# Optimization experiments

Measured on AMD Instinct MI355X. Metric: run time of the kernel, lower is better.

Reference implementation:

```python
import jax, jax.numpy as jnp
import numpy as np

B, S, H, NH, DK = 128, 512, 1000, 8, 125
LN_EPS = 1e-5


def setup_inputs() -> dict:
    key = jax.random.key(0)
    ks = jax.random.split(key, 12)
    s = 1.0 / np.sqrt(H)
    inp = {
        "q": jax.random.normal(ks[0], (B, S, H), jnp.float32),
        "k": jax.random.normal(ks[1], (B, S, H), jnp.float32),
        "v": jax.random.normal(ks[2], (B, S, H), jnp.float32),
        "mask": jax.random.randint(ks[3], (B, 1, 1, S), 0, 2) > 0,
        "Wq_w": jax.random.normal(ks[4], (H, H), jnp.float32) * s,
        "Wq_b": jnp.zeros((H,), jnp.float32),
        "Wk_w": jax.random.normal(ks[5], (H, H), jnp.float32) * s,
        "Wk_b": jnp.zeros((H,), jnp.float32),
        "Wv_w": jax.random.normal(ks[6], (H, H), jnp.float32) * s,
        "Wv_b": jnp.zeros((H,), jnp.float32),
        "Wo_w": jax.random.normal(ks[7], (H, H), jnp.float32) * s,
        "Wo_b": jnp.zeros((H,), jnp.float32),
        "ln_g": jnp.ones((H,), jnp.float32),
        "ln_b": jnp.zeros((H,), jnp.float32),
    }
    return inp


def _layernorm(x, g, b):
    mu = jnp.mean(x, -1, keepdims=True)
    var = jnp.mean(jnp.square(x - mu), -1, keepdims=True)
    return (x - mu) * jax.lax.rsqrt(var + LN_EPS) * g + b


def reference(q, k, v, mask, Wq_w, Wq_b, Wk_w, Wk_b, Wv_w, Wv_b, Wo_w, Wo_b, ln_g, ln_b):
    x = q
    # projections: torch Linear is x @ W.T + b
    qh = (q @ Wq_w.T + Wq_b).reshape(B, S, NH, DK).transpose(0, 2, 1, 3)  # [B,NH,S,DK]
    kh = (k @ Wk_w.T + Wk_b).reshape(B, S, NH, DK).transpose(0, 2, 1, 3)
    vh = (v @ Wv_w.T + Wv_b).reshape(B, S, NH, DK).transpose(0, 2, 1, 3)
    scores = jnp.einsum("bhqd,bhkd->bhqk", qh, kh) / np.sqrt(DK)  # [B,NH,S,S]
    scores = jnp.where(mask, jnp.float32(-10000.0), scores)
    a = jax.nn.softmax(scores, axis=-1)
    z = jnp.einsum("bhqk,bhkd->bhqd", a, vh)  # [B,NH,S,DK]
    z = z.transpose(0, 2, 1, 3).reshape(B, S, NH * DK)
    z = z @ Wo_w.T + Wo_b
    # dropout is identity in eval mode
    return _layernorm(x + z, ln_g, ln_b)
```

## Files before the change

### kernel.cpp

```cpp
#include <hip/hip_runtime.h>


typedef unsigned short u16;
typedef short short8 __attribute__((ext_vector_type(8)));
typedef float f32x4 __attribute__((ext_vector_type(8/2)));

#define XQ_E 0ull
#define XK_E 67108864ull
#define XV_E 134217728ull
#define WQ_E 201326592ull
#define WK_E 202375168ull
#define WV_E 203423744ull
#define WO_E 204472320ull
#define QH_E 205520896ull
#define KH_E 272629760ull
#define VT_E 339738624ull
#define Z2_E 0ull
#define Y_BYTE 134217728ull

__device__ __forceinline__ u16 f2bf(float f) {
  unsigned u = __float_as_uint(f);
  u += 0x7fffu + ((u >> 16) & 1u);
  return (u16)(u >> 16);
}

__device__ __forceinline__ void gl_lds16(const void* g, void* l) {
  __builtin_amdgcn_global_load_lds((const __attribute__((address_space(1))) void*)g,
                                   (__attribute__((address_space(3))) void*)l,
                                   16, 0, 0);
}

__global__ __launch_bounds__(128) void cvt_kernel(
    const float* __restrict__ q, const float* __restrict__ k, const float* __restrict__ v,
    const float* __restrict__ wq, const float* __restrict__ wk,
    const float* __restrict__ wv, const float* __restrict__ wo,
    u16* __restrict__ ws16) {
  const int row = blockIdx.x;
  const int c0 = threadIdx.x * 8;
  const float* src;
  u16* dst;
  bool valid;
  if (row < 196608) {
    const int m = row >> 16, r = row & 65535;
    src = (m == 0 ? q : (m == 1 ? k : v)) + (size_t)r * 1000;
    dst = ws16 + (size_t)m * 67108864ull + (size_t)r * 1024;
    valid = (c0 < 1000);
  } else {
    const int t2 = row - 196608;
    const int wm = t2 >> 10, r = t2 & 1023;
    const float* W = (wm == 0 ? wq : (wm == 1 ? wk : (wm == 2 ? wv : wo)));
    src = W + (size_t)r * 1000;
    dst = ws16 + WQ_E + (size_t)wm * 1048576ull + (size_t)r * 1024;
    valid = (c0 < 1000) && (r < 1000);
  }
  short8 o = {0, 0, 0, 0, 0, 0, 0, 0};
  if (valid) {
    float4 a = *(const float4*)(src + c0);
    float4 b = *(const float4*)(src + c0 + 4);
    o[0] = (short)f2bf(a.x); o[1] = (short)f2bf(a.y);
    o[2] = (short)f2bf(a.z); o[3] = (short)f2bf(a.w);
    o[4] = (short)f2bf(b.x); o[5] = (short)f2bf(b.y);
    o[6] = (short)f2bf(b.z); o[7] = (short)f2bf(b.w);
  }
  *(short8*)(dst + c0) = o;
}

__global__ __launch_bounds__(256) void zpad_kernel(u16* __restrict__ ws16) {
  const int r = blockIdx.x * 256 + threadIdx.x;
  u16* p = ws16 + KH_E + (size_t)r * 128 + 125;
  p[0] = 0; p[1] = 0; p[2] = 0;
}

__global__ __launch_bounds__(256, 2) void gemm_bt(
    u16* __restrict__ ws16,
    const float* __restrict__ bq, const float* __restrict__ bk,
    const float* __restrict__ bv, const float* __restrict__ bo,
    const float* __restrict__ qres, int mode_base) {
  const int mode = mode_base + blockIdx.z;
  const u16* A; const u16* Bw; const float* bias;
  if (mode == 0)      { A = ws16 + XQ_E; Bw = ws16 + WQ_E; bias = bq; }
  else if (mode == 1) { A = ws16 + XK_E; Bw = ws16 + WK_E; bias = bk; }
  else if (mode == 2) { A = ws16 + XV_E; Bw = ws16 + WV_E; bias = bv; }
  else                { A = ws16 + Z2_E; Bw = ws16 + WO_E; bias = bo; }

  __shared__ __attribute__((aligned(16))) u16 lA[128 * 64];
  __shared__ __attribute__((aligned(16))) u16 lB[128 * 64];

  const int tid = threadIdx.x;
  const int w = tid >> 6, lane = tid & 63;
  const int m0 = blockIdx.x * 128, n0 = blockIdx.y * 128;

  const f32x4 zz = {0.f, 0.f, 0.f, 0.f};
  f32x4 acc[4][4];
#pragma unroll
  for (int mi = 0; mi < 4; ++mi)
#pragma unroll
    for (int ni = 0; ni < 4; ++ni) acc[mi][ni] = zz;

  const int srow = lane >> 3;
  const int scol = (lane & 7) * 8;
  const int wm = (w >> 1) * 64, wn = (w & 1) * 64;
  const int fr = lane & 15, quad = lane >> 4, fq = quad * 8;

  for (int kt = 0; kt < 16; ++kt) {
    __syncthreads();
    const int k0 = kt * 64;
#pragma unroll
    for (int i = 0; i < 4; ++i) {
      const int rbase = w * 32 + i * 8;
      gl_lds16(A  + (size_t)(m0 + rbase + srow) * 1024 + k0 + scol, (void*)(lA + rbase * 64));
      gl_lds16(Bw + (size_t)(n0 + rbase + srow) * 1024 + k0 + scol, (void*)(lB + rbase * 64));
    }
    __syncthreads();
#pragma unroll
    for (int ks = 0; ks < 2; ++ks) {
      short8 af[4], bf[4];
#pragma unroll
      for (int mi = 0; mi < 4; ++mi)
        af[mi] = *(const short8*)(lA + (wm + mi * 16 + fr) * 64 + ks * 32 + fq);
#pragma unroll
      for (int ni = 0; ni < 4; ++ni)
        bf[ni] = *(const short8*)(lB + (wn + ni * 16 + fr) * 64 + ks * 32 + fq);
#pragma unroll
      for (int mi = 0; mi < 4; ++mi)
#pragma unroll
        for (int ni = 0; ni < 4; ++ni)
          acc[mi][ni] = __builtin_amdgcn_mfma_f32_16x16x32_bf16(af[mi], bf[ni], acc[mi][ni], 0, 0, 0);
    }
  }

#pragma unroll
  for (int mi = 0; mi < 4; ++mi)
#pragma unroll
    for (int ni = 0; ni < 4; ++ni)
#pragma unroll
      for (int r = 0; r < 4; ++r) {
        const int gr = m0 + wm + mi * 16 + quad * 4 + r;
        const int gc = n0 + wn + ni * 16 + fr;
        if (gc >= 1000) continue;
        float val = acc[mi][ni][r] + bias[gc];
        if (mode <= 1) {
          if (mode == 0) val *= 0.08944271909999159f;
          const int head = gc / 125, dk = gc - head * 125;
          const int b = gr >> 9, s = gr & 511;
          u16* dst = ws16 + (mode == 0 ? QH_E : KH_E);
          dst[((size_t)((b * 8 + head) * 512 + s)) * 128 + dk] = f2bf(val);
        } else if (mode == 2) {
          const int head = gc / 125, dk = gc - head * 125;
          const int b = gr >> 9, s = gr & 511;
          ws16[VT_E + ((size_t)((b * 8 + head) * 128 + dk)) * 512 + s] = f2bf(val);
        } else {
          float* Y = (float*)((char*)ws16 + Y_BYTE);
          Y[(size_t)gr * 1000 + gc] = val + qres[(size_t)gr * 1000 + gc];
        }
      }
}

__global__ __launch_bounds__(256, 2) void attn_kernel(
    u16* __restrict__ ws16, const int* __restrict__ maskp) {
  const u16* QH = ws16 + QH_E;
  const u16* KH = ws16 + KH_E;
  const u16* VT = ws16 + VT_E;
  u16* Z2 = ws16 + Z2_E;

  const int qt = blockIdx.x, bnh = blockIdx.y;
  const int b = bnh >> 3, head = bnh & 7;
  const int tid = threadIdx.x, w = tid >> 6, lane = tid & 63;
  const int fr = lane & 15, quad = lane >> 4, fq = quad * 8;

  __shared__ __attribute__((aligned(16))) u16 lQ[64 * 128];
  __shared__ __attribute__((aligned(16))) u16 lKV[64 * 128];
  __shared__ __attribute__((aligned(16))) u16 lP[4][16 * 72];
  __shared__ float lM[512];

  {
    const int* mp = maskp + b * 512;
    lM[tid] = mp[tid] ? 1.0f : 0.0f;
    lM[tid + 256] = mp[tid + 256] ? 1.0f : 0.0f;
  }
  {
    const int lrow = lane >> 4, lc = (lane & 15) * 8;
#pragma unroll
    for (int i = 0; i < 4; ++i) {
      const int rbase = w * 16 + i * 4;
      gl_lds16(QH + ((size_t)(bnh * 512 + qt * 64 + rbase + lrow)) * 128 + lc,
               (void*)(lQ + rbase * 128));
    }
  }
  __syncthreads();

  short8 af[4];
#pragma unroll
  for (int ks = 0; ks < 4; ++ks)
    af[ks] = *(const short8*)(lQ + (w * 16 + fr) * 128 + ks * 32 + fq);

  const f32x4 zz = {0.f, 0.f, 0.f, 0.f};
  f32x4 sA[32];
#pragma unroll
  for (int i = 0; i < 32; ++i) sA[i] = zz;

#pragma unroll
  for (int kt = 0; kt < 8; ++kt) {
    __syncthreads();
    {
      const int lrow = lane >> 4, lc = (lane & 15) * 8;
#pragma unroll
      for (int i = 0; i < 4; ++i) {
        const int rbase = w * 16 + i * 4;
        gl_lds16(KH + ((size_t)(bnh * 512 + kt * 64 + rbase + lrow)) * 128 + lc,
                 (void*)(lKV + rbase * 128));
      }
    }
    __syncthreads();
#pragma unroll
    for (int ks = 0; ks < 4; ++ks)
#pragma unroll
      for (int n = 0; n < 4; ++n) {
        short8 bf = *(const short8*)(lKV + (n * 16 + fr) * 128 + ks * 32 + fq);
        sA[kt * 4 + n] = __builtin_amdgcn_mfma_f32_16x16x32_bf16(af[ks], bf, sA[kt * 4 + n], 0, 0, 0);
      }
  }

  float linv[4];
#pragma unroll
  for (int r = 0; r < 4; ++r) {
    float mr = -3.0e38f;
#pragma unroll
    for (int ct = 0; ct < 32; ++ct) {
      float vv = sA[ct][r];
      vv = (lM[ct * 16 + fr] != 0.0f) ? -10000.0f : vv;
      sA[ct][r] = vv;
      mr = fmaxf(mr, vv);
    }
    mr = fmaxf(mr, __shfl_xor(mr, 1, 64));
    mr = fmaxf(mr, __shfl_xor(mr, 2, 64));
    mr = fmaxf(mr, __shfl_xor(mr, 4, 64));
    mr = fmaxf(mr, __shfl_xor(mr, 8, 64));
    float lr = 0.f;
#pragma unroll
    for (int ct = 0; ct < 32; ++ct) {
      float p = __expf(sA[ct][r] - mr);
      sA[ct][r] = p;
      lr += p;
    }
    lr += __shfl_xor(lr, 1, 64);
    lr += __shfl_xor(lr, 2, 64);
    lr += __shfl_xor(lr, 4, 64);
    lr += __shfl_xor(lr, 8, 64);
    linv[r] = 1.0f / lr;
  }

  f32x4 zA[8];
#pragma unroll
  for (int n = 0; n < 8; ++n) zA[n] = zz;
  u16* myP = lP[w];

#pragma unroll
  for (int kt = 0; kt < 8; ++kt) {
    __syncthreads();
    {
      const int lrow = lane >> 3, lc = (lane & 7) * 8;
#pragma unroll
      for (int i = 0; i < 4; ++i) {
        const int rbase = w * 32 + i * 8;
        gl_lds16(VT + ((size_t)(bnh * 128 + rbase + lrow)) * 512 + kt * 64 + lc,
                 (void*)(lKV + rbase * 64));
      }
    }
    __syncthreads();
#pragma unroll
    for (int n = 0; n < 4; ++n)
#pragma unroll
      for (int r = 0; r < 4; ++r)
        myP[(quad * 4 + r) * 72 + n * 16 + fr] = f2bf(sA[kt * 4 + n][r]);
#pragma unroll
    for (int ks = 0; ks < 2; ++ks) {
      short8 ap = *(const short8*)(myP + fr * 72 + ks * 32 + fq);
#pragma unroll
      for (int n = 0; n < 8; ++n) {
        short8 bv = *(const short8*)(lKV + (n * 16 + fr) * 64 + ks * 32 + fq);
        zA[n] = __builtin_amdgcn_mfma_f32_16x16x32_bf16(ap, bv, zA[n], 0, 0, 0);
      }
    }
  }

#pragma unroll
  for (int n = 0; n < 8; ++n)
#pragma unroll
    for (int r = 0; r < 4; ++r) {
      const int dk = n * 16 + fr;
      if (dk < 125) {
        const int sg = qt * 64 + w * 16 + quad * 4 + r;
        const float val = zA[n][r] * linv[r];
        Z2[((size_t)(b * 512 + sg)) * 1024 + head * 125 + dk] = f2bf(val);
      }
    }
}

__global__ __launch_bounds__(256) void ln_kernel(
    const float* __restrict__ Y, const float* __restrict__ g,
    const float* __restrict__ be, float* __restrict__ out) {
  const size_t row = blockIdx.x;
  const int t = threadIdx.x;
  const float* yr = Y + row * 1000;
  float4 x = make_float4(0.f, 0.f, 0.f, 0.f);
  if (t < 250) x = *(const float4*)(yr + t * 4);
  float s1 = x.x + x.y + x.z + x.w;
  float s2 = x.x * x.x + x.y * x.y + x.z * x.z + x.w * x.w;
#pragma unroll
  for (int off = 1; off < 64; off <<= 1) {
    s1 += __shfl_xor(s1, off, 64);
    s2 += __shfl_xor(s2, off, 64);
  }
  __shared__ float r1[4], r2[4];
  const int w = t >> 6, lane = t & 63;
  if (lane == 0) { r1[w] = s1; r2[w] = s2; }
  __syncthreads();
  const float S1 = r1[0] + r1[1] + r1[2] + r1[3];
  const float S2 = r2[0] + r2[1] + r2[2] + r2[3];
  const float mu = S1 * 0.001f;
  const float var = S2 * 0.001f - mu * mu;
  const float rstd = rsqrtf(var + 1e-5f);
  if (t < 250) {
    float4 gg = *(const float4*)(g + t * 4);
    float4 bb = *(const float4*)(be + t * 4);
    float4 o;
    o.x = (x.x - mu) * rstd * gg.x + bb.x;
    o.y = (x.y - mu) * rstd * gg.y + bb.y;
    o.z = (x.z - mu) * rstd * gg.z + bb.z;
    o.w = (x.w - mu) * rstd * gg.w + bb.w;
    *(float4*)(out + row * 1000 + t * 4) = o;
  }
}

extern "C" void kernel_launch(void* const* d_in, const int* in_sizes, int n_in,
                              void* d_out, int out_size, void* d_ws, size_t ws_size,
                              hipStream_t stream) {
  const float* q   = (const float*)d_in[0];
  const float* k   = (const float*)d_in[1];
  const float* v   = (const float*)d_in[2];
  const int*   mk  = (const int*)  d_in[3];
  const float* wqw = (const float*)d_in[4];
  const float* wqb = (const float*)d_in[5];
  const float* wkw = (const float*)d_in[6];
  const float* wkb = (const float*)d_in[7];
  const float* wvw = (const float*)d_in[8];
  const float* wvb = (const float*)d_in[9];
  const float* wow = (const float*)d_in[10];
  const float* wob = (const float*)d_in[11];
  const float* lng = (const float*)d_in[12];
  const float* lnb = (const float*)d_in[13];
  u16* ws16 = (u16*)d_ws;

  cvt_kernel<<<dim3(200704), dim3(128), 0, stream>>>(q, k, v, wqw, wkw, wvw, wow, ws16);
  zpad_kernel<<<dim3(2048), dim3(256), 0, stream>>>(ws16);
  gemm_bt<<<dim3(512, 8, 3), dim3(256), 0, stream>>>(ws16, wqb, wkb, wvb, wob, q, 0);
  attn_kernel<<<dim3(8, 1024), dim3(256), 0, stream>>>(ws16, mk);
  gemm_bt<<<dim3(512, 8, 1), dim3(256), 0, stream>>>(ws16, wqb, wkb, wvb, wob, q, 3);
  ln_kernel<<<dim3(65536), dim3(256), 0, stream>>>(
      (const float*)((const char*)d_ws + Y_BYTE), lng, lnb, (float*)d_out);
}
```

Measured before the change: 2.481 ms.

## Rewrite projection GEMM with 256x256 tiles, double-buffered swizzled LDS and prefetch

The projection GEMM moves from 128x128 tiles with 256 threads to 256x256 tiles with 512 threads. LDS is double-buffered, global-to-LDS loads for the next K step are interleaved with MFMA work using explicit waitcnt and barriers, and LDS uses an XOR swizzle to avoid bank conflicts. Block indices are remapped so neighbouring blocks share tiles, which should improve L2 reuse. The goal is to hide load latency and raise MFMA utilisation, at the cost of much more LDS (128 KB per block), more registers for accumulators, and fragile hand-tuned vmcnt counts.

```diff
diff --git a/kernel.cpp b/kernel.cpp
--- a/kernel.cpp
+++ b/kernel.cpp
@@ -3,7 +3,7 @@
 
 typedef unsigned short u16;
 typedef short short8 __attribute__((ext_vector_type(8)));
-typedef float f32x4 __attribute__((ext_vector_type(8/2)));
+typedef float f32x4 __attribute__((ext_vector_type(4)));
 
 #define XQ_E 0ull
 #define XK_E 67108864ull
@@ -71,7 +71,7 @@
   p[0] = 0; p[1] = 0; p[2] = 0;
 }
 
-__global__ __launch_bounds__(256, 2) void gemm_bt(
+__global__ __launch_bounds__(512, 2) void gemm_bt(
     u16* __restrict__ ws16,
     const float* __restrict__ bq, const float* __restrict__ bk,
     const float* __restrict__ bv, const float* __restrict__ bo,
@@ -83,60 +83,111 @@
   else if (mode == 2) { A = ws16 + XV_E; Bw = ws16 + WV_E; bias = bv; }
   else                { A = ws16 + Z2_E; Bw = ws16 + WO_E; bias = bo; }
 
-  __shared__ __attribute__((aligned(16))) u16 lA[128 * 64];
-  __shared__ __attribute__((aligned(16))) u16 lB[128 * 64];
+  __shared__ __attribute__((aligned(16))) u16 lA[2][256 * 64];
+  __shared__ __attribute__((aligned(16))) u16 lB[2][256 * 64];
 
   const int tid = threadIdx.x;
-  const int w = tid >> 6, lane = tid & 63;
-  const int m0 = blockIdx.x * 128, n0 = blockIdx.y * 128;
+  const int wid = tid >> 6, lane = tid & 63;
+  const int wr = wid >> 2, wc = wid & 3;
+  const int fr = lane & 15, quad = lane >> 4;
+  const int widl = wid * 512;
+
+  const int f = blockIdx.x;
+  const int logical = (f & 7) * 128 + (f >> 3);
+  const int mt = logical >> 2, nt = logical & 3;
+  const int m0 = mt * 256, n0 = nt * 256;
+
+  const int r8 = tid >> 3;
+  const int swz_cb = ((tid & 7) * 16) ^ ((r8 & 7) << 4);
+  const char* srcA = (const char*)(A + (size_t)m0 * 1024) + (size_t)r8 * 2048 + swz_cb;
+  const char* srcB = (const char*)(Bw + (size_t)n0 * 1024) + (size_t)r8 * 2048 + swz_cb;
+
+  auto stA = [&](int b2, int q, int kb) {
+    gl_lds16(srcA + (size_t)q * 131072 + kb, (void*)(&lA[b2][q * 4096 + widl]));
+  };
+  auto stB = [&](int b2, int q, int kb) {
+    gl_lds16(srcB + (size_t)q * 131072 + kb, (void*)(&lB[b2][q * 4096 + widl]));
+  };
 
   const f32x4 zz = {0.f, 0.f, 0.f, 0.f};
-  f32x4 acc[4][4];
-#pragma unroll
-  for (int mi = 0; mi < 4; ++mi)
+  f32x4 acc[8][4];
+#pragma unroll
+  for (int mi = 0; mi < 8; ++mi)
 #pragma unroll
     for (int ni = 0; ni < 4; ++ni) acc[mi][ni] = zz;
 
-  const int srow = lane >> 3;
-  const int scol = (lane & 7) * 8;
-  const int wm = (w >> 1) * 64, wn = (w & 1) * 64;
-  const int fr = lane & 15, quad = lane >> 4, fq = quad * 8;
-
-  for (int kt = 0; kt < 16; ++kt) {
-    __syncthreads();
-    const int k0 = kt * 64;
-#pragma unroll
-    for (int i = 0; i < 4; ++i) {
-      const int rbase = w * 32 + i * 8;
-      gl_lds16(A  + (size_t)(m0 + rbase + srow) * 1024 + k0 + scol, (void*)(lA + rbase * 64));
-      gl_lds16(Bw + (size_t)(n0 + rbase + srow) * 1024 + k0 + scol, (void*)(lB + rbase * 64));
-    }
-    __syncthreads();
-#pragma unroll
-    for (int ks = 0; ks < 2; ++ks) {
-      short8 af[4], bf[4];
-#pragma unroll
-      for (int mi = 0; mi < 4; ++mi)
-        af[mi] = *(const short8*)(lA + (wm + mi * 16 + fr) * 64 + ks * 32 + fq);
-#pragma unroll
-      for (int ni = 0; ni < 4; ++ni)
-        bf[ni] = *(const short8*)(lB + (wn + ni * 16 + fr) * 64 + ks * 32 + fq);
-#pragma unroll
-      for (int mi = 0; mi < 4; ++mi)
+  stB(0, 0, 0); stB(0, 1, 0); stB(0, 2, 0); stB(0, 3, 0);
+  stA(0, 0, 0); stA(0, 2, 0); stA(0, 1, 0); stA(0, 3, 0);
+  asm volatile("s_waitcnt vmcnt(2)" ::: "memory");
+  asm volatile("s_barrier" ::: "memory");
+
+  const int rowA = (wr * 128 + fr) * 128;
+  const int rowB = (wc * 64 + fr) * 128;
+  const int swr = (fr & 7) << 4;
+
+  short8 bfr[4][2];
+
+#pragma unroll 2
+  for (int t = 0; t < 16; ++t) {
+    const int buf = t & 1, nb = buf ^ 1;
+    const char* tA = (const char*)(&lA[buf][0]);
+    const char* tB = (const char*)(&lB[buf][0]);
+    const int kb = (t + 1) * 128;
+    const bool pf = (t < 15);
+
+#pragma unroll
+    for (int p = 0; p < 4; ++p) {
+      short8 afr[2][2];
+#pragma unroll
+      for (int j = 0; j < 2; ++j)
+#pragma unroll
+        for (int ks = 0; ks < 2; ++ks)
+          afr[j][ks] = *(const short8*)(tA + rowA + (p * 2 + j) * 2048 +
+                                        ((ks * 64 + quad * 16) ^ swr));
+      if (p == 0) {
 #pragma unroll
         for (int ni = 0; ni < 4; ++ni)
-          acc[mi][ni] = __builtin_amdgcn_mfma_f32_16x16x32_bf16(af[mi], bf[ni], acc[mi][ni], 0, 0, 0);
-    }
-  }
-
-#pragma unroll
-  for (int mi = 0; mi < 4; ++mi)
+#pragma unroll
+          for (int ks = 0; ks < 2; ++ks)
+            bfr[ni][ks] = *(const short8*)(tB + rowB + ni * 2048 +
+                                           ((ks * 64 + quad * 16) ^ swr));
+      }
+      if (pf) {
+        if (p == 0)      { stB(nb, 0, kb); stB(nb, 1, kb); }
+        else if (p == 1) { stB(nb, 2, kb); stB(nb, 3, kb); }
+        else if (p == 2) { stA(nb, 0, kb); stA(nb, 2, kb); }
+        else             { stA(nb, 1, kb); stA(nb, 3, kb); }
+      }
+      asm volatile("s_barrier" ::: "memory");
+      asm volatile("s_waitcnt lgkmcnt(0)" ::: "memory");
+      __builtin_amdgcn_s_setprio(1);
+#pragma unroll
+      for (int j = 0; j < 2; ++j)
+#pragma unroll
+        for (int ks = 0; ks < 2; ++ks)
+#pragma unroll
+          for (int ni = 0; ni < 4; ++ni)
+            acc[p * 2 + j][ni] = __builtin_amdgcn_mfma_f32_16x16x32_bf16(
+                afr[j][ks], bfr[ni][ks], acc[p * 2 + j][ni], 0, 0, 0);
+      __builtin_amdgcn_s_setprio(0);
+      if (p == 1) {
+        if (pf) asm volatile("s_waitcnt vmcnt(4)" ::: "memory");
+        else    asm volatile("s_waitcnt vmcnt(0)" ::: "memory");
+      } else if (p == 3 && pf) {
+        asm volatile("s_waitcnt vmcnt(2)" ::: "memory");
+      }
+      asm volatile("s_barrier" ::: "memory");
+    }
+  }
+
+#pragma unroll
+  for (int mi = 0; mi < 8; ++mi)
 #pragma unroll
     for (int ni = 0; ni < 4; ++ni)
 #pragma unroll
       for (int r = 0; r < 4; ++r) {
-        const int gr = m0 + wm + mi * 16 + quad * 4 + r;
-        const int gc = n0 + wn + ni * 16 + fr;
+        const int gr = m0 + wr * 128 + mi * 16 + quad * 4 + r;
+        const int gc = n0 + wc * 64 + ni * 16 + fr;
         if (gc >= 1000) continue;
         float val = acc[mi][ni][r] + bias[gc];
         if (mode <= 1) {
@@ -354,9 +405,9 @@
 
   cvt_kernel<<<dim3(200704), dim3(128), 0, stream>>>(q, k, v, wqw, wkw, wvw, wow, ws16);
   zpad_kernel<<<dim3(2048), dim3(256), 0, stream>>>(ws16);
-  gemm_bt<<<dim3(512, 8, 3), dim3(256), 0, stream>>>(ws16, wqb, wkb, wvb, wob, q, 0);
+  gemm_bt<<<dim3(1024, 1, 3), dim3(512), 0, stream>>>(ws16, wqb, wkb, wvb, wob, q, 0);
   attn_kernel<<<dim3(8, 1024), dim3(256), 0, stream>>>(ws16, mk);
-  gemm_bt<<<dim3(512, 8, 1), dim3(256), 0, stream>>>(ws16, wqb, wkb, wvb, wob, q, 3);
+  gemm_bt<<<dim3(1024, 1, 1), dim3(512), 0, stream>>>(ws16, wqb, wkb, wvb, wob, q, 3);
   ln_kernel<<<dim3(65536), dim3(256), 0, stream>>>(
       (const float*)((const char*)d_ws + Y_BYTE), lng, lnb, (float*)d_out);
 }
```

Result: no change. 2.434 ms (-1.9%).
